# Optimization experiments

Measured on AMD Instinct MI355X. Metric: run time of the kernel, lower is better.

Reference implementation:

```python
import jax, jax.numpy as jnp
import numpy as np

B, N, FEAT, MSG, LINK_H, CLS = 8, 128, 1024, 256, 512, 600
PROP = 2  # propagate_layers


def setup_inputs() -> dict:
    key = jax.random.key(0)
    ks = jax.random.split(key, 16)
    g = lambda k, shape, s=0.02: jax.random.normal(k, shape, dtype=jnp.float32) * s
    inp = {
        'edge_features': g(ks[0], (B, N, N, FEAT), 1.0),
        'node_features': g(ks[1], (B, N, FEAT), 1.0),
        'adj_mat': jnp.zeros((B, N, N), jnp.float32),          # shape placeholder only
        'node_labels': jnp.zeros((B, N, CLS), jnp.float32),    # shape placeholder only
        'human_nums': 64,
        'obj_nums': 64,
        # feature resize linears (Linear(FEAT -> MSG))
        'W_er': g(ks[2], (MSG, FEAT)), 'b_er': jnp.zeros((MSG,), jnp.float32),
        'W_nr': g(ks[3], (MSG, FEAT)), 'b_nr': jnp.zeros((MSG,), jnp.float32),
        # link fun (GraphConv): 1x1 Conv2d(MSG->LINK_H), ReLU, 1x1 Conv2d(LINK_H->1)
        'W_l1': g(ks[4], (LINK_H, MSG)), 'b_l1': jnp.zeros((LINK_H,), jnp.float32),
        'W_l2': g(ks[5], (1, LINK_H)), 'b_l2': jnp.zeros((1,), jnp.float32),
        # message fun linear_concat_relu: Linear(node+edge = 2*MSG -> MSG), ReLU
        'W_m': g(ks[6], (MSG, 2 * MSG)), 'b_m': jnp.zeros((MSG,), jnp.float32),
        # GRU(input=MSG, hidden=MSG), single layer single step
        'W_ih': g(ks[7], (3 * MSG, MSG)), 'b_ih': jnp.zeros((3 * MSG,), jnp.float32),
        'W_hh': g(ks[8], (3 * MSG, MSG)), 'b_hh': jnp.zeros((3 * MSG,), jnp.float32),
        # readout fc: Linear(MSG -> CLS)
        'W_r': g(ks[9], (CLS, MSG)), 'b_r': jnp.zeros((CLS,), jnp.float32),
    }
    return inp


def reference(edge_features, node_features, adj_mat, node_labels,
              human_nums, obj_nums,
              W_er, b_er, W_nr, b_nr, W_l1, b_l1, W_l2, b_l2,
              W_m, b_m, W_ih, b_ih, W_hh, b_hh, W_r, b_r):
    # valid_node_num = human_nums + obj_nums == N for every batch element.
    # Resize raw features to message size.
    e = edge_features @ W_er.T + b_er        # [B, v, w, MSG]
    h = node_features @ W_nr.T + b_nr        # [B, w, MSG]  (node states are never rewritten in source)
    # Split concat-linear into two matmuls to avoid materializing [B,N,N,2*MSG].
    W_mh, W_me = W_m[:, :MSG], W_m[:, MSG:]
    msg_h = jnp.einsum('bwd,md->bwm', h, W_mh)                 # node part, shared over target v
    msg_e = jnp.einsum('bvwd,md->bvwm', e, W_me) + b_m          # edge part (original e, constant over rounds)
    edge_state = e
    m = None
    pred_adj = None
    for _ in range(PROP):
        # link fun: per-(v,w) MLP over channels (1x1 convs)
        x = jax.nn.relu(edge_state @ W_l1.T + b_l1)             # [B,v,w,LINK_H]
        pred_adj = (x @ W_l2.T + b_l2)[..., 0]                  # [B,N,N]
        sig = jax.nn.sigmoid(pred_adj)
        # message fun linear_concat_relu, gated by predicted adjacency
        m = jax.nn.relu(msg_h[:, None, :, :] + msg_e)           # [B,v,w,MSG]
        m = sig[..., None] * m
        # hidden_edge_states[round+1][:, :, w, v] = m_v[:, :, w]
        edge_state = jnp.swapaxes(m, 1, 2)
    # node update happens per node each round but hidden node states are never
    # written back in the source, so only the last round's GRU step matters.
    m_sum = m.sum(axis=2)                                       # [B,v,MSG]
    gi = m_sum @ W_ih.T + b_ih
    gh = h @ W_hh.T + b_hh
    ir, iz, inn = jnp.split(gi, 3, axis=-1)
    hr, hz, hn = jnp.split(gh, 3, axis=-1)
    r = jax.nn.sigmoid(ir + hr)
    z = jax.nn.sigmoid(iz + hz)
    n = jnp.tanh(inn + r * hn)
    h_new = (1.0 - z) * n + z * h                               # [B,N,MSG]
    pred_node_labels = h_new @ W_r.T + b_r                      # [B,N,CLS]
    return pred_adj, pred_node_labels
```

## Files before the change

### kernel.cpp

```cpp
#include <hip/hip_runtime.h>
#include <cstdint>
#include <cstddef>

#define NND   128
#define FEATD 1024
#define MSGD  256
#define LHD   512
#define CLSD  600
#define LDST  264

typedef __bf16 bf16_t;
typedef bf16_t bf16x8 __attribute__((ext_vector_type(8)));
typedef float  f32x4  __attribute__((ext_vector_type(4)));
typedef unsigned short u16;
typedef u16 u16x8 __attribute__((ext_vector_type(8)));
typedef u16 u16x4 __attribute__((ext_vector_type(4)));

static __device__ __forceinline__ float bf2f(u16 u) {
  union { unsigned u; float f; } x; x.u = ((unsigned)u) << 16; return x.f;
}
static __device__ __forceinline__ u16 f2bf(float f) {
  union { float f; unsigned u; } x; x.f = f;
  return (u16)((x.u + 0x7fffu + ((x.u >> 16) & 1u)) >> 16);
}
static __device__ __forceinline__ f32x4 mfma16(u16x8 a, u16x8 b, f32x4 c) {
  return __builtin_amdgcn_mfma_f32_16x16x32_bf16(
      __builtin_bit_cast(bf16x8, a), __builtin_bit_cast(bf16x8, b), c, 0, 0, 0);
}
static __device__ __forceinline__ f32x4 zero4() {
  f32x4 v; v[0] = 0.f; v[1] = 0.f; v[2] = 0.f; v[3] = 0.f; return v;
}
static __device__ __forceinline__ float sigm(float x) { return 1.0f / (1.0f + expf(-x)); }

__global__ void k_cvt(const float* __restrict__ src, u16* __restrict__ dst, int n) {
  int i = (blockIdx.x * 256 + threadIdx.x) * 4;
  if (i + 3 < n) {
    float4 f = *(const float4*)(src + i);
    u16x4 o; o[0] = f2bf(f.x); o[1] = f2bf(f.y); o[2] = f2bf(f.z); o[3] = f2bf(f.w);
    *(u16x4*)(dst + i) = o;
  }
}

__global__ __launch_bounds__(256) void k_comb(const float* __restrict__ Wm,
                                              const float* __restrict__ Wer,
                                              const float* __restrict__ b_er,
                                              const float* __restrict__ b_m,
                                              u16* __restrict__ WcombB,
                                              float* __restrict__ bcomb) {
  const int m = blockIdx.x >> 2, ch = blockIdx.x & 3;
  const int d = ch * 256 + threadIdx.x;
  float s = 0.f;
  for (int k = 0; k < 256; ++k)
    s += Wm[(size_t)m * 512 + 256 + k] * Wer[(size_t)k * FEATD + d];
  WcombB[(size_t)m * FEATD + d] = f2bf(s);
  if (ch == 0 && threadIdx.x == 0) {
    float bb2 = b_m[m];
    for (int k = 0; k < 256; ++k) bb2 += Wm[(size_t)m * 512 + 256 + k] * b_er[k];
    bcomb[m] = bb2;
  }
}

__global__ __launch_bounds__(256) void s1_hmsg(const float* __restrict__ node,
                                               const float* __restrict__ Wnr,
                                               const float* __restrict__ bnr,
                                               const float* __restrict__ Wm,
                                               float* __restrict__ h32,
                                               u16* __restrict__ msghB) {
  __shared__ float nrow[FEATD];
  __shared__ float hrow[MSGD];
  const int r = blockIdx.x;
  const int t = threadIdx.x;
  *(float4*)(&nrow[t * 4]) = *(const float4*)(node + (size_t)r * FEATD + t * 4);
  __syncthreads();
  float acc = bnr[t];
  for (int d = 0; d < FEATD; ++d) acc += nrow[d] * Wnr[(size_t)t * FEATD + d];
  h32[(size_t)r * MSGD + t] = acc;
  hrow[t] = acc;
  __syncthreads();
  float mh = 0.f;
  for (int k = 0; k < MSGD; ++k) mh += hrow[k] * Wm[(size_t)t * 2 * MSGD + k];
  msghB[(size_t)r * MSGD + t] = f2bf(mh);
}

__global__ __launch_bounds__(256, 2) void k_main(
    const float* __restrict__ edge, const u16* __restrict__ Wer, const u16* __restrict__ Wm,
    const u16* __restrict__ Wl1, const float* __restrict__ b_er, const float* __restrict__ b_m,
    const float* __restrict__ b_l1, const float* __restrict__ W_l2, const float* __restrict__ b_l2,
    const u16* __restrict__ msgh, u16* __restrict__ M0g, float* __restrict__ pa_out) {
  __shared__ __align__(16) u16 lsE[64][LDST];
  __shared__ __align__(16) u16 lsM[64][LDST];
  __shared__ float lsPA[4][64];
  __shared__ float lsSig[64];

  const int tid = threadIdx.x, lane = tid & 63, wave = tid >> 6;
  const int lh = lane & 15, lq = lane >> 4;
  const int base = blockIdx.x * 64;
  const int bb = base >> 14, vv = (base >> 7) & 127, w0 = base & 127;

  f32x4 acc[4][4];
#pragma unroll
  for (int m = 0; m < 4; ++m)
#pragma unroll
    for (int t = 0; t < 4; ++t) acc[m][t] = zero4();

  const int srow = tid >> 2;
  const int scq  = (tid & 3) * 16;
  const float* esrc = edge + (size_t)(base + srow) * FEATD + scq;
  float4 lda[4], ldb[4];

  auto LOADS_A = [&](int s) {
#pragma unroll
    for (int i = 0; i < 4; ++i) lda[i] = *(const float4*)(esrc + s * 64 + i * 4);
  };
  auto LOADS_B = [&](int s) {
#pragma unroll
    for (int i = 0; i < 4; ++i) ldb[i] = *(const float4*)(esrc + s * 64 + i * 4);
  };
  auto WRITES = [&](const float4* ld, int slot) {
    u16* wp = &lsE[srow][slot * 64 + scq];
    u16x8 o0, o1;
    o0[0] = f2bf(ld[0].x); o0[1] = f2bf(ld[0].y); o0[2] = f2bf(ld[0].z); o0[3] = f2bf(ld[0].w);
    o0[4] = f2bf(ld[1].x); o0[5] = f2bf(ld[1].y); o0[6] = f2bf(ld[1].z); o0[7] = f2bf(ld[1].w);
    o1[0] = f2bf(ld[2].x); o1[1] = f2bf(ld[2].y); o1[2] = f2bf(ld[2].z); o1[3] = f2bf(ld[2].w);
    o1[4] = f2bf(ld[3].x); o1[5] = f2bf(ld[3].y); o1[6] = f2bf(ld[3].z); o1[7] = f2bf(ld[3].w);
    *(u16x8*)wp = o0;
    *(u16x8*)(wp + 8) = o1;
  };
  auto MSTEP = [&](int sk, int slot) {
#pragma unroll
    for (int ks = 0; ks < 2; ++ks) {
      u16x8 afr[4];
#pragma unroll
      for (int m = 0; m < 4; ++m)
        afr[m] = *(const u16x8*)(&lsE[16 * m + lh][slot * 64 + ks * 32 + lq * 8]);
      const int kg = sk * 64 + ks * 32 + lq * 8;
#pragma unroll
      for (int t = 0; t < 4; ++t) {
        int col = wave * 64 + t * 16 + lh;
        u16x8 bfr = *(const u16x8*)(Wer + (size_t)col * FEATD + kg);
#pragma unroll
        for (int m = 0; m < 4; ++m) acc[m][t] = mfma16(afr[m], bfr, acc[m][t]);
      }
    }
  };

  LOADS_A(0);
  LOADS_B(1);
  for (int s2 = 0; s2 < 16; s2 += 2) {
    WRITES(lda, 0);
    if (s2 + 2 < 16) LOADS_A(s2 + 2);
    __syncthreads();
    MSTEP(s2, 0);
    WRITES(ldb, 1);
    if (s2 + 3 < 16) LOADS_B(s2 + 3);
    __syncthreads();
    MSTEP(s2 + 1, 1);
  }
  __syncthreads();
#pragma unroll
  for (int t = 0; t < 4; ++t) {
    int col = wave * 64 + t * 16 + lh;
    float be = b_er[col];
#pragma unroll
    for (int m = 0; m < 4; ++m)
#pragma unroll
      for (int j = 0; j < 4; ++j)
        lsE[16 * m + 4 * lq + j][col] = f2bf(acc[m][t][j] + be);
  }
  __syncthreads();

  float prow[4][4];
#pragma unroll
  for (int m = 0; m < 4; ++m)
#pragma unroll
    for (int j = 0; j < 4; ++j) prow[m][j] = 0.f;
#pragma unroll
  for (int np = 0; np < 2; ++np) {
#pragma unroll
    for (int m = 0; m < 4; ++m)
#pragma unroll
      for (int t = 0; t < 4; ++t) acc[m][t] = zero4();
#pragma unroll
    for (int ks = 0; ks < 8; ++ks) {
      u16x8 afr[4];
#pragma unroll
      for (int m = 0; m < 4; ++m) afr[m] = *(const u16x8*)(&lsE[16 * m + lh][ks * 32 + lq * 8]);
      const int kg = ks * 32 + lq * 8;
#pragma unroll
      for (int t = 0; t < 4; ++t) {
        int col = wave * 128 + np * 64 + t * 16 + lh;
        u16x8 bfr = *(const u16x8*)(Wl1 + (size_t)col * MSGD + kg);
#pragma unroll
        for (int m = 0; m < 4; ++m) acc[m][t] = mfma16(afr[m], bfr, acc[m][t]);
      }
    }
#pragma unroll
    for (int t = 0; t < 4; ++t) {
      int col = wave * 128 + np * 64 + t * 16 + lh;
      float bl = b_l1[col], wl = W_l2[col];
#pragma unroll
      for (int m = 0; m < 4; ++m)
#pragma unroll
        for (int j = 0; j < 4; ++j) prow[m][j] += fmaxf(acc[m][t][j] + bl, 0.f) * wl;
    }
  }
#pragma unroll
  for (int off = 1; off < 16; off <<= 1)
#pragma unroll
    for (int m = 0; m < 4; ++m)
#pragma unroll
      for (int j = 0; j < 4; ++j) prow[m][j] += __shfl_xor(prow[m][j], off, 64);
  if (lh == 0) {
#pragma unroll
    for (int m = 0; m < 4; ++m)
#pragma unroll
      for (int j = 0; j < 4; ++j) lsPA[wave][16 * m + 4 * lq + j] = prow[m][j];
  }
  __syncthreads();
  if (tid < 64) {
    float pa1 = lsPA[0][tid] + lsPA[1][tid] + lsPA[2][tid] + lsPA[3][tid] + b_l2[0];
    lsSig[tid] = sigm(pa1);
  }
#pragma unroll
  for (int i = 0; i < 8; ++i) {
    int idx = tid + i * 256;
    int row = idx >> 5;
    int c8 = (idx & 31) << 3;
    *(u16x8*)(&lsM[row][c8]) =
        *(const u16x8*)(msgh + (size_t)(bb * NND + w0 + row) * MSGD + c8);
  }
  __syncthreads();

#pragma unroll
  for (int m = 0; m < 4; ++m)
#pragma unroll
    for (int t = 0; t < 4; ++t) acc[m][t] = zero4();
#pragma unroll
  for (int ks = 0; ks < 8; ++ks) {
    u16x8 afr[4];
#pragma unroll
    for (int m = 0; m < 4; ++m) afr[m] = *(const u16x8*)(&lsE[16 * m + lh][ks * 32 + lq * 8]);
    const int kg = ks * 32 + lq * 8;
#pragma unroll
    for (int t = 0; t < 4; ++t) {
      int col = wave * 64 + t * 16 + lh;
      u16x8 bfr = *(const u16x8*)(Wm + (size_t)col * 512 + 256 + kg);
#pragma unroll
      for (int m = 0; m < 4; ++m) acc[m][t] = mfma16(afr[m], bfr, acc[m][t]);
    }
  }
#pragma unroll
  for (int t = 0; t < 4; ++t) {
    int col = wave * 64 + t * 16 + lh;
    float bm = b_m[col];
#pragma unroll
    for (int m = 0; m < 4; ++m)
#pragma unroll
      for (int j = 0; j < 4; ++j) {
        int row = 16 * m + 4 * lq + j;
        float mh = bf2f(lsM[row][col]);
        lsM[row][col] = f2bf(fmaxf(acc[m][t][j] + bm + mh, 0.f));
      }
  }
  __syncthreads();
#pragma unroll
  for (int i = 0; i < 8; ++i) {
    int idx = tid + i * 256;
    int row = idx >> 5;
    int c8 = (idx & 31) << 3;
    u16x8 m0v = *(const u16x8*)(&lsM[row][c8]);
    if (M0g) *(u16x8*)(M0g + (size_t)(base + row) * MSGD + c8) = m0v;
    float s = lsSig[row];
    u16x8 sc;
#pragma unroll
    for (int j = 0; j < 8; ++j) sc[j] = f2bf(bf2f(m0v[j]) * s);
    *(u16x8*)(&lsM[row][c8]) = sc;
  }
  __syncthreads();

#pragma unroll
  for (int m = 0; m < 4; ++m)
#pragma unroll
    for (int j = 0; j < 4; ++j) prow[m][j] = 0.f;
#pragma unroll
  for (int np = 0; np < 2; ++np) {
#pragma unroll
    for (int m = 0; m < 4; ++m)
#pragma unroll
      for (int t = 0; t < 4; ++t) acc[m][t] = zero4();
#pragma unroll
    for (int ks = 0; ks < 8; ++ks) {
      u16x8 afr[4];
#pragma unroll
      for (int m = 0; m < 4; ++m) afr[m] = *(const u16x8*)(&lsM[16 * m + lh][ks * 32 + lq * 8]);
      const int kg = ks * 32 + lq * 8;
#pragma unroll
      for (int t = 0; t < 4; ++t) {
        int col = wave * 128 + np * 64 + t * 16 + lh;
        u16x8 bfr = *(const u16x8*)(Wl1 + (size_t)col * MSGD + kg);
#pragma unroll
        for (int m = 0; m < 4; ++m) acc[m][t] = mfma16(afr[m], bfr, acc[m][t]);
      }
    }
#pragma unroll
    for (int t = 0; t < 4; ++t) {
      int col = wave * 128 + np * 64 + t * 16 + lh;
      float bl = b_l1[col], wl = W_l2[col];
#pragma unroll
      for (int m = 0; m < 4; ++m)
#pragma unroll
        for (int j = 0; j < 4; ++j) prow[m][j] += fmaxf(acc[m][t][j] + bl, 0.f) * wl;
    }
  }
#pragma unroll
  for (int off = 1; off < 16; off <<= 1)
#pragma unroll
    for (int m = 0; m < 4; ++m)
#pragma unroll
      for (int j = 0; j < 4; ++j) prow[m][j] += __shfl_xor(prow[m][j], off, 64);
  if (lh == 0) {
#pragma unroll
    for (int m = 0; m < 4; ++m)
#pragma unroll
      for (int j = 0; j < 4; ++j) lsPA[wave][16 * m + 4 * lq + j] = prow[m][j];
  }
  __syncthreads();
  if (tid < 64) {
    float q = lsPA[0][tid] + lsPA[1][tid] + lsPA[2][tid] + lsPA[3][tid] + b_l2[0];
    size_t o = ((size_t)bb * NND + (w0 + tid)) * NND + vv;
    pa_out[o] = q;
  }
}

__global__ __launch_bounds__(256) void k_msum_lite(const u16* __restrict__ M0g,
                                                   const float* __restrict__ qv,
                                                   float* __restrict__ msum) {
  __shared__ float sig[128];
  const int bv = blockIdx.x, tid = threadIdx.x;
  if (tid < 128) sig[tid] = sigm(qv[(size_t)bv * NND + tid]);
  __syncthreads();
  const u16* p = M0g + (size_t)bv * NND * MSGD + tid;
  float a = 0.f;
#pragma unroll 8
  for (int w = 0; w < 128; ++w) a += sig[w] * bf2f(p[(size_t)w * MSGD]);
  msum[(size_t)bv * MSGD + tid] = a;
}

__global__ __launch_bounds__(256, 2) void k_msum2(
    const float* __restrict__ edge, const u16* __restrict__ Wcomb,
    const float* __restrict__ bcomb, const u16* __restrict__ msgh,
    const float* __restrict__ qv, float* __restrict__ msum) {
  __shared__ __align__(16) u16 lsE[64][LDST];
  __shared__ __align__(16) u16 lsM[64][LDST];
  __shared__ float lsSig[64];
  const int tid = threadIdx.x, lane = tid & 63, wave = tid >> 6;
  const int lh = lane & 15, lq = lane >> 4;
  const int bv = blockIdx.x;
  const int bb = bv >> 7;

  float csum[4] = {0.f, 0.f, 0.f, 0.f};

  for (int hh = 0; hh < 2; ++hh) {
    if (tid < 64) lsSig[tid] = sigm(qv[(size_t)bv * NND + hh * 64 + tid]);
#pragma unroll
    for (int i = 0; i < 8; ++i) {
      int idx = tid + i * 256;
      int row = idx >> 5;
      int c8 = (idx & 31) << 3;
      *(u16x8*)(&lsM[row][c8]) =
          *(const u16x8*)(msgh + (size_t)(bb * NND + hh * 64 + row) * MSGD + c8);
    }
    f32x4 acc[4][4];
#pragma unroll
    for (int m = 0; m < 4; ++m)
#pragma unroll
      for (int t = 0; t < 4; ++t) acc[m][t] = zero4();

    for (int kc = 0; kc < 4; ++kc) {
#pragma unroll
      for (int i = 0; i < 16; ++i) {
        int idx = tid + i * 256;
        int row = idx >> 6;
        int c4 = (idx & 63) << 2;
        float4 f = *(const float4*)(edge + (size_t)(bv * NND + hh * 64 + row) * FEATD + kc * 256 + c4);
        u16x4 o; o[0] = f2bf(f.x); o[1] = f2bf(f.y); o[2] = f2bf(f.z); o[3] = f2bf(f.w);
        *(u16x4*)(&lsE[row][c4]) = o;
      }
      __syncthreads();
#pragma unroll
      for (int ks = 0; ks < 8; ++ks) {
        u16x8 afr[4];
#pragma unroll
        for (int m = 0; m < 4; ++m) afr[m] = *(const u16x8*)(&lsE[16 * m + lh][ks * 32 + lq * 8]);
        const int kg = kc * 256 + ks * 32 + lq * 8;
#pragma unroll
        for (int t = 0; t < 4; ++t) {
          int col = wave * 64 + t * 16 + lh;
          u16x8 bfr = *(const u16x8*)(Wcomb + (size_t)col * FEATD + kg);
#pragma unroll
          for (int m = 0; m < 4; ++m) acc[m][t] = mfma16(afr[m], bfr, acc[m][t]);
        }
      }
      __syncthreads();
    }
#pragma unroll
    for (int t = 0; t < 4; ++t) {
      int col = wave * 64 + t * 16 + lh;
      float bc = bcomb[col];
#pragma unroll
      for (int m = 0; m < 4; ++m)
#pragma unroll
        for (int j = 0; j < 4; ++j) {
          int row = 16 * m + 4 * lq + j;
          float m0 = fmaxf(acc[m][t][j] + bc + bf2f(lsM[row][col]), 0.f);
          csum[t] += lsSig[row] * m0;
        }
    }
    __syncthreads();
  }
#pragma unroll
  for (int off = 16; off < 64; off <<= 1)
#pragma unroll
    for (int t = 0; t < 4; ++t) csum[t] += __shfl_xor(csum[t], off, 64);
  if (lq == 0) {
#pragma unroll
    for (int t = 0; t < 4; ++t)
      msum[(size_t)bv * MSGD + wave * 64 + t * 16 + lh] = csum[t];
  }
}

__global__ __launch_bounds__(256) void k_gru(const float* __restrict__ msum,
                                             const float* __restrict__ h32,
                                             const float* __restrict__ Wih, const float* __restrict__ bih,
                                             const float* __restrict__ Whh, const float* __restrict__ bhh,
                                             const float* __restrict__ Wr, const float* __restrict__ br,
                                             float* __restrict__ outlab) {
  __shared__ __align__(16) float sM[8][256];
  __shared__ __align__(16) float sH[8][256];
  __shared__ __align__(16) float sHn[8][256];
  const int tid = threadIdx.x;
  const int r0 = blockIdx.x * 8;
#pragma unroll
  for (int i = 0; i < 2; ++i) {
    int idx = tid + i * 256;
    int row = idx >> 6;
    int c = (idx & 63) << 2;
    *(float4*)(&sM[row][c]) = *(const float4*)(msum + (size_t)(r0 + row) * 256 + c);
    *(float4*)(&sH[row][c]) = *(const float4*)(h32 + (size_t)(r0 + row) * 256 + c);
  }
  __syncthreads();
  float gi[3][8], gh[3][8];
#pragma unroll
  for (int c = 0; c < 3; ++c) {
    float bi_ = bih[tid + 256 * c], bh_ = bhh[tid + 256 * c];
#pragma unroll
    for (int rr = 0; rr < 8; ++rr) { gi[c][rr] = bi_; gh[c][rr] = bh_; }
  }
  for (int k = 0; k < 256; k += 4) {
    float4 wi[3], wh[3];
#pragma unroll
    for (int c = 0; c < 3; ++c) {
      wi[c] = *(const float4*)(Wih + (size_t)(tid + 256 * c) * 256 + k);
      wh[c] = *(const float4*)(Whh + (size_t)(tid + 256 * c) * 256 + k);
    }
#pragma unroll
    for (int rr = 0; rr < 8; ++rr) {
      float4 ms = *(const float4*)(&sM[rr][k]);
      float4 hh = *(const float4*)(&sH[rr][k]);
#pragma unroll
      for (int c = 0; c < 3; ++c) {
        gi[c][rr] += wi[c].x * ms.x + wi[c].y * ms.y + wi[c].z * ms.z + wi[c].w * ms.w;
        gh[c][rr] += wh[c].x * hh.x + wh[c].y * hh.y + wh[c].z * hh.z + wh[c].w * hh.w;
      }
    }
  }
#pragma unroll
  for (int rr = 0; rr < 8; ++rr) {
    float r = sigm(gi[0][rr] + gh[0][rr]);
    float z = sigm(gi[1][rr] + gh[1][rr]);
    float n = tanhf(gi[2][rr] + r * gh[2][rr]);
    sHn[rr][tid] = (1.f - z) * n + z * sH[rr][tid];
  }
  __syncthreads();
  float lab[3][8];
  int cs[3]; bool has[3];
#pragma unroll
  for (int c = 0; c < 3; ++c) {
    cs[c] = tid + 256 * c;
    has[c] = cs[c] < CLSD;
    float b0 = has[c] ? br[cs[c]] : 0.f;
#pragma unroll
    for (int rr = 0; rr < 8; ++rr) lab[c][rr] = b0;
  }
  for (int k = 0; k < 256; k += 4) {
    float4 wr[3];
#pragma unroll
    for (int c = 0; c < 3; ++c) {
      if (has[c]) wr[c] = *(const float4*)(Wr + (size_t)cs[c] * 256 + k);
      else { wr[c].x = 0.f; wr[c].y = 0.f; wr[c].z = 0.f; wr[c].w = 0.f; }
    }
#pragma unroll
    for (int rr = 0; rr < 8; ++rr) {
      float4 hv = *(const float4*)(&sHn[rr][k]);
#pragma unroll
      for (int c = 0; c < 3; ++c)
        lab[c][rr] += wr[c].x * hv.x + wr[c].y * hv.y + wr[c].z * hv.z + wr[c].w * hv.w;
    }
  }
#pragma unroll
  for (int c = 0; c < 3; ++c) {
    if (has[c]) {
#pragma unroll
      for (int rr = 0; rr < 8; ++rr)
        outlab[(size_t)(r0 + rr) * CLSD + cs[c]] = lab[c][rr];
    }
  }
}

extern "C" void kernel_launch(void* const* d_in, const int* in_sizes, int n_in,
                              void* d_out, int out_size, void* d_ws, size_t ws_size,
                              hipStream_t stream) {
  const float* edge = (const float*)d_in[0];
  const float* node = (const float*)d_in[1];
  const float* W_er = (const float*)d_in[6];
  const float* b_er = (const float*)d_in[7];
  const float* W_nr = (const float*)d_in[8];
  const float* b_nr = (const float*)d_in[9];
  const float* W_l1 = (const float*)d_in[10];
  const float* b_l1 = (const float*)d_in[11];
  const float* W_l2 = (const float*)d_in[12];
  const float* b_l2 = (const float*)d_in[13];
  const float* W_m  = (const float*)d_in[14];
  const float* b_m  = (const float*)d_in[15];
  const float* W_ih = (const float*)d_in[16];
  const float* b_ih = (const float*)d_in[17];
  const float* W_hh = (const float*)d_in[18];
  const float* b_hh = (const float*)d_in[19];
  const float* W_r  = (const float*)d_in[20];
  const float* b_r  = (const float*)d_in[21];

  char* ws = (char*)d_ws;
  size_t off = 0;
  auto alloc = [&](size_t bytes) -> void* {
    void* p = ws + off;
    off += (bytes + 511) & ~(size_t)511;
    return p;
  };
  u16* WerB     = (u16*)alloc((size_t)262144 * 2);
  u16* WmB      = (u16*)alloc((size_t)131072 * 2);
  u16* Wl1B     = (u16*)alloc((size_t)131072 * 2);
  u16* WcombB   = (u16*)alloc((size_t)262144 * 2);
  float* bcombF = (float*)alloc((size_t)256 * 4);
  u16* msghB    = (u16*)alloc((size_t)262144 * 2);
  float* h32    = (float*)alloc((size_t)262144 * 4);
  float* msum   = (float*)alloc((size_t)262144 * 4);
  u16* M0g      = (u16*)alloc((size_t)33554432 * 2);
  size_t off_m0 = off;
  const bool fast = (ws_size >= off_m0);
  u16* M0arg = fast ? M0g : (u16*)nullptr;

  float* out_pa  = (float*)d_out;
  float* out_lab = out_pa + 131072;

  k_cvt  <<<256,  256, 0, stream>>>(W_er, WerB, 262144);
  k_cvt  <<<128,  256, 0, stream>>>(W_m,  WmB,  131072);
  k_cvt  <<<128,  256, 0, stream>>>(W_l1, Wl1B, 131072);
  s1_hmsg<<<1024, 256, 0, stream>>>(node, W_nr, b_nr, W_m, h32, msghB);
  if (!fast)
    k_comb<<<1024, 256, 0, stream>>>(W_m, W_er, b_er, b_m, WcombB, bcombF);

  k_main<<<2048, 256, 0, stream>>>(edge, WerB, WmB, Wl1B, b_er, b_m, b_l1, W_l2, b_l2,
                                   msghB, M0arg, out_pa);
  if (fast)
    k_msum_lite<<<1024, 256, 0, stream>>>(M0g, out_pa, msum);
  else
    k_msum2<<<1024, 256, 0, stream>>>(edge, WcombB, bcombF, msghB, out_pa, msum);
  k_gru<<<128, 256, 0, stream>>>(msum, h32, W_ih, b_ih, W_hh, b_hh, W_r, b_r, out_lab);
}
```

Baseline: 715.3 us.

## Move node resize and message-h to MFMA kernels, transpose GRU weights, vectorize msum

Replaces the scalar per-row node resize and msg_h kernel with two bf16 MFMA GEMM kernels, converting W_nr to bf16 first. The GRU/readout weights are pre-transposed so each thread reads coalesced columns instead of strided rows. The msum reduction now uses 16-byte vector loads with an LDS partial-sum combine. These target the small side kernels around the main edge kernel. They add extra conversion launches and bf16 rounding of h for msg_h.

After: 806.1 us. 1.13x slower.

```diff
diff --git a/kernel.cpp b/kernel.cpp
--- a/kernel.cpp
+++ b/kernel.cpp
@@ -38,6 +38,27 @@
     float4 f = *(const float4*)(src + i);
     u16x4 o; o[0] = f2bf(f.x); o[1] = f2bf(f.y); o[2] = f2bf(f.z); o[3] = f2bf(f.w);
     *(u16x4*)(dst + i) = o;
+  }
+}
+
+__global__ __launch_bounds__(256) void k_cvtT(const float* __restrict__ in,
+                                              float* __restrict__ out, int R) {
+  __shared__ float tile[32][33];
+  const int tx = threadIdx.x & 31, ty = threadIdx.x >> 5;
+  const int tr = blockIdx.x >> 3, tc = blockIdx.x & 7;
+#pragma unroll
+  for (int i = 0; i < 4; ++i) {
+    int r = tr * 32 + ty + i * 8;
+    if (r < R) tile[ty + i * 8][tx] = in[(size_t)r * 256 + tc * 32 + tx];
+  }
+  __syncthreads();
+  const int r = tr * 32 + tx;
+  if (r < R) {
+#pragma unroll
+    for (int i = 0; i < 4; ++i) {
+      int c = tc * 32 + ty + i * 8;
+      out[(size_t)c * R + r] = tile[tx][ty + i * 8];
+    }
   }
 }
 
@@ -60,29 +81,114 @@
   }
 }
 
-__global__ __launch_bounds__(256) void s1_hmsg(const float* __restrict__ node,
-                                               const float* __restrict__ Wnr,
-                                               const float* __restrict__ bnr,
-                                               const float* __restrict__ Wm,
-                                               float* __restrict__ h32,
-                                               u16* __restrict__ msghB) {
-  __shared__ float nrow[FEATD];
-  __shared__ float hrow[MSGD];
-  const int r = blockIdx.x;
-  const int t = threadIdx.x;
-  *(float4*)(&nrow[t * 4]) = *(const float4*)(node + (size_t)r * FEATD + t * 4);
-  __syncthreads();
-  float acc = bnr[t];
-  for (int d = 0; d < FEATD; ++d) acc += nrow[d] * Wnr[(size_t)t * FEATD + d];
-  h32[(size_t)r * MSGD + t] = acc;
-  hrow[t] = acc;
-  __syncthreads();
-  float mh = 0.f;
-  for (int k = 0; k < MSGD; ++k) mh += hrow[k] * Wm[(size_t)t * 2 * MSGD + k];
-  msghB[(size_t)r * MSGD + t] = f2bf(mh);
-}
-
-__global__ __launch_bounds__(256, 2) void k_main(
+__global__ __launch_bounds__(256) void k_h(const float* __restrict__ node,
+                                           const u16* __restrict__ Wnr,
+                                           const float* __restrict__ bnr,
+                                           float* __restrict__ h32,
+                                           u16* __restrict__ hbf) {
+  __shared__ __align__(16) u16 lsA[64][LDST];
+  const int tid = threadIdx.x, lane = tid & 63, wave = tid >> 6;
+  const int lh = lane & 15, lq = lane >> 4;
+  const int base = blockIdx.x * 64;
+
+  f32x4 acc[4][4];
+#pragma unroll
+  for (int m = 0; m < 4; ++m)
+#pragma unroll
+    for (int t = 0; t < 4; ++t) acc[m][t] = zero4();
+
+  for (int kc = 0; kc < 4; ++kc) {
+#pragma unroll
+    for (int i = 0; i < 16; ++i) {
+      int idx = tid + i * 256;
+      int row = idx >> 6;
+      int c4 = (idx & 63) << 2;
+      float4 f = *(const float4*)(node + (size_t)(base + row) * FEATD + kc * 256 + c4);
+      u16x4 o; o[0] = f2bf(f.x); o[1] = f2bf(f.y); o[2] = f2bf(f.z); o[3] = f2bf(f.w);
+      *(u16x4*)(&lsA[row][c4]) = o;
+    }
+    __syncthreads();
+#pragma unroll
+    for (int ks = 0; ks < 8; ++ks) {
+      u16x8 afr[4];
+#pragma unroll
+      for (int m = 0; m < 4; ++m) afr[m] = *(const u16x8*)(&lsA[16 * m + lh][ks * 32 + lq * 8]);
+      const int kg = kc * 256 + ks * 32 + lq * 8;
+#pragma unroll
+      for (int t = 0; t < 4; ++t) {
+        int col = wave * 64 + t * 16 + lh;
+        u16x8 bfr = *(const u16x8*)(Wnr + (size_t)col * FEATD + kg);
+#pragma unroll
+        for (int m = 0; m < 4; ++m) acc[m][t] = mfma16(afr[m], bfr, acc[m][t]);
+      }
+    }
+    __syncthreads();
+  }
+#pragma unroll
+  for (int t = 0; t < 4; ++t) {
+    int col = wave * 64 + t * 16 + lh;
+    float be = bnr[col];
+#pragma unroll
+    for (int m = 0; m < 4; ++m)
+#pragma unroll
+      for (int j = 0; j < 4; ++j) {
+        int row = 16 * m + 4 * lq + j;
+        float v = acc[m][t][j] + be;
+        size_t o = (size_t)(base + row) * MSGD + col;
+        h32[o] = v; hbf[o] = f2bf(v);
+      }
+  }
+}
+
+__global__ __launch_bounds__(256) void k_msgh(const u16* __restrict__ hbf,
+                                              const u16* __restrict__ Wm,
+                                              u16* __restrict__ msgh) {
+  __shared__ __align__(16) u16 lsA[64][LDST];
+  const int tid = threadIdx.x, lane = tid & 63, wave = tid >> 6;
+  const int lh = lane & 15, lq = lane >> 4;
+  const int base = blockIdx.x * 64;
+
+#pragma unroll
+  for (int i = 0; i < 8; ++i) {
+    int idx = tid + i * 256;
+    int row = idx >> 5;
+    int c8 = (idx & 31) << 3;
+    *(u16x8*)(&lsA[row][c8]) = *(const u16x8*)(hbf + (size_t)(base + row) * MSGD + c8);
+  }
+  __syncthreads();
+  f32x4 acc[4][4];
+#pragma unroll
+  for (int m = 0; m < 4; ++m)
+#pragma unroll
+    for (int t = 0; t < 4; ++t) acc[m][t] = zero4();
+#pragma unroll
+  for (int ks = 0; ks < 8; ++ks) {
+    u16x8 afr[4];
+#pragma unroll
+    for (int m = 0; m < 4; ++m) afr[m] = *(const u16x8*)(&lsA[16 * m + lh][ks * 32 + lq * 8]);
+    const int kg = ks * 32 + lq * 8;
+#pragma unroll
+    for (int t = 0; t < 4; ++t) {
+      int col = wave * 64 + t * 16 + lh;
+      u16x8 bfr = *(const u16x8*)(Wm + (size_t)col * 512 + kg);
+#pragma unroll
+      for (int m = 0; m < 4; ++m) acc[m][t] = mfma16(afr[m], bfr, acc[m][t]);
+    }
+  }
+#pragma unroll
+  for (int t = 0; t < 4; ++t) {
+    int col = wave * 64 + t * 16 + lh;
+#pragma unroll
+    for (int m = 0; m < 4; ++m)
+#pragma unroll
+      for (int j = 0; j < 4; ++j) {
+        int row = 16 * m + 4 * lq + j;
+        msgh[(size_t)(base + row) * MSGD + col] = f2bf(acc[m][t][j]);
+      }
+  }
+}
+
+__global__ __launch_bounds__(256, 2) void k_main_full(
     const float* __restrict__ edge, const u16* __restrict__ Wer, const u16* __restrict__ Wm,
     const u16* __restrict__ Wl1, const float* __restrict__ b_er, const float* __restrict__ b_m,
     const float* __restrict__ b_l1, const float* __restrict__ W_l2, const float* __restrict__ b_l2,
@@ -336,14 +442,28 @@
                                                    const float* __restrict__ qv,
                                                    float* __restrict__ msum) {
   __shared__ float sig[128];
+  __shared__ __align__(16) float part[8][256];
   const int bv = blockIdx.x, tid = threadIdx.x;
   if (tid < 128) sig[tid] = sigm(qv[(size_t)bv * NND + tid]);
   __syncthreads();
-  const u16* p = M0g + (size_t)bv * NND * MSGD + tid;
-  float a = 0.f;
-#pragma unroll 8
-  for (int w = 0; w < 128; ++w) a += sig[w] * bf2f(p[(size_t)w * MSGD]);
-  msum[(size_t)bv * MSGD + tid] = a;
+  const int cg = (tid & 31) * 8, rg = tid >> 5;
+  float a[8];
+#pragma unroll
+  for (int j = 0; j < 8; ++j) a[j] = 0.f;
+  for (int i = 0; i < 16; ++i) {
+    int row = rg + i * 8;
+    u16x8 v = *(const u16x8*)(M0g + ((size_t)bv * NND + row) * MSGD + cg);
+    float s = sig[row];
+#pragma unroll
+    for (int j = 0; j < 8; ++j) a[j] += s * bf2f(v[j]);
+  }
+#pragma unroll
+  for (int j = 0; j < 8; ++j) part[rg][cg + j] = a[j];
+  __syncthreads();
+  float r = 0.f;
+#pragma unroll
+  for (int g = 0; g < 8; ++g) r += part[g][tid];
+  msum[(size_t)bv * MSGD + tid] = r;
 }
 
 __global__ __launch_bounds__(256, 2) void k_msum2(
@@ -429,12 +549,15 @@
   }
 }
 
-__global__ __launch_bounds__(256) void k_gru(const float* __restrict__ msum,
-                                             const float* __restrict__ h32,
-                                             const float* __restrict__ Wih, const float* __restrict__ bih,
-                                             const float* __restrict__ Whh, const float* __restrict__ bhh,
-                                             const float* __restrict__ Wr, const float* __restrict__ br,
-                                             float* __restrict__ outlab) {
+__global__ __launch_bounds__(256) void k_gru_t(const float* __restrict__ msum,
+                                               const float* __restrict__ h32,
+                                               const float* __restrict__ WihT,
+                                               const float* __restrict__ bih,
+                                               const float* __restrict__ WhhT,
+                                               const float* __restrict__ bhh,
+                                               const float* __restrict__ WrT,
+                                               const float* __restrict__ br,
+                                               float* __restrict__ outlab) {
   __shared__ __align__(16) float sM[8][256];
   __shared__ __align__(16) float sH[8][256];
   __shared__ __align__(16) float sHn[8][256];
@@ -456,22 +579,18 @@
 #pragma unroll
     for (int rr = 0; rr < 8; ++rr) { gi[c][rr] = bi_; gh[c][rr] = bh_; }
   }
-  for (int k = 0; k < 256; k += 4) {
-    float4 wi[3], wh[3];
-#pragma unroll
-    for (int c = 0; c < 3; ++c) {
-      wi[c] = *(const float4*)(Wih + (size_t)(tid + 256 * c) * 256 + k);
-      wh[c] = *(const float4*)(Whh + (size_t)(tid + 256 * c) * 256 + k);
-    }
+  for (int k = 0; k < 256; ++k) {
+    float wi0 = WihT[(size_t)k * 768 + tid];
+    float wi1 = WihT[(size_t)k * 768 + 256 + tid];
+    float wi2 = WihT[(size_t)k * 768 + 512 + tid];
+    float wh0 = WhhT[(size_t)k * 768 + tid];
+    float wh1 = WhhT[(size_t)k * 768 + 256 + tid];
+    float wh2 = WhhT[(size_t)k * 768 + 512 + tid];
 #pragma unroll
     for (int rr = 0; rr < 8; ++rr) {
-      float4 ms = *(const float4*)(&sM[rr][k]);
-      float4 hh = *(const float4*)(&sH[rr][k]);
-#pragma unroll
-      for (int c = 0; c < 3; ++c) {
-        gi[c][rr] += wi[c].x * ms.x + wi[c].y * ms.y + wi[c].z * ms.z + wi[c].w * ms.w;
-        gh[c][rr] += wh[c].x * hh.x + wh[c].y * hh.y + wh[c].z * hh.z + wh[c].w * hh.w;
-      }
+      float ms = sM[rr][k], hh = sH[rr][k];
+      gi[0][rr] += wi0 * ms; gi[1][rr] += wi1 * ms; gi[2][rr] += wi2 * ms;
+      gh[0][rr] += wh0 * hh; gh[1][rr] += wh1 * hh; gh[2][rr] += wh2 * hh;
     }
   }
 #pragma unroll
@@ -483,37 +602,30 @@
   }
   __syncthreads();
   float lab[3][8];
-  int cs[3]; bool has[3];
+  const bool has2 = (tid + 512) < CLSD;
 #pragma unroll
   for (int c = 0; c < 3; ++c) {
-    cs[c] = tid + 256 * c;
-    has[c] = cs[c] < CLSD;
-    float b0 = has[c] ? br[cs[c]] : 0.f;
+    int cs = tid + 256 * c;
+    float b0 = (c < 2 || has2) ? br[cs < CLSD ? cs : 0] : 0.f;
+    if (c < 2) b0 = br[cs];
 #pragma unroll
     for (int rr = 0; rr < 8; ++rr) lab[c][rr] = b0;
   }
-  for (int k = 0; k < 256; k += 4) {
-    float4 wr[3];
-#pragma unroll
-    for (int c = 0; c < 3; ++c) {
-      if (has[c]) wr[c] = *(const float4*)(Wr + (size_t)cs[c] * 256 + k);
-      else { wr[c].x = 0.f; wr[c].y = 0.f; wr[c].z = 0.f; wr[c].w = 0.f; }
-    }
+  for (int k = 0; k < 256; ++k) {
+    float w0 = WrT[(size_t)k * CLSD + tid];
+    float w1 = WrT[(size_t)k * CLSD + 256 + tid];
+    float w2 = has2 ? WrT[(size_t)k * CLSD + 512 + tid] : 0.f;
 #pragma unroll
     for (int rr = 0; rr < 8; ++rr) {
-      float4 hv = *(const float4*)(&sHn[rr][k]);
-#pragma unroll
-      for (int c = 0; c < 3; ++c)
-        lab[c][rr] += wr[c].x * hv.x + wr[c].y * hv.y + wr[c].z * hv.z + wr[c].w * hv.w;
-    }
-  }
-#pragma unroll
-  for (int c = 0; c < 3; ++c) {
-    if (has[c]) {
-#pragma unroll
-      for (int rr = 0; rr < 8; ++rr)
-        outlab[(size_t)(r0 + rr) * CLSD + cs[c]] = lab[c][rr];
-    }
+      float hv = sHn[rr][k];
+      lab[0][rr] += w0 * hv; lab[1][rr] += w1 * hv; lab[2][rr] += w2 * hv;
+    }
+  }
+#pragma unroll
+  for (int rr = 0; rr < 8; ++rr) {
+    outlab[(size_t)(r0 + rr) * CLSD + tid] = lab[0][rr];
+    outlab[(size_t)(r0 + rr) * CLSD + 256 + tid] = lab[1][rr];
+    if (has2) outlab[(size_t)(r0 + rr) * CLSD + 512 + tid] = lab[2][rr];
   }
 }
 
@@ -547,13 +659,18 @@
     return p;
   };
   u16* WerB     = (u16*)alloc((size_t)262144 * 2);
+  u16* WnrB     = (u16*)alloc((size_t)262144 * 2);
   u16* WmB      = (u16*)alloc((size_t)131072 * 2);
   u16* Wl1B     = (u16*)alloc((size_t)131072 * 2);
   u16* WcombB   = (u16*)alloc((size_t)262144 * 2);
   float* bcombF = (float*)alloc((size_t)256 * 4);
   u16* msghB    = (u16*)alloc((size_t)262144 * 2);
+  u16* hB       = (u16*)alloc((size_t)262144 * 2);
   float* h32    = (float*)alloc((size_t)262144 * 4);
   float* msum   = (float*)alloc((size_t)262144 * 4);
+  float* WihT   = (float*)alloc((size_t)196608 * 4);
+  float* WhhT   = (float*)alloc((size_t)196608 * 4);
+  float* WrT    = (float*)alloc((size_t)153600 * 4);
   u16* M0g      = (u16*)alloc((size_t)33554432 * 2);
   size_t off_m0 = off;
   const bool fast = (ws_size >= off_m0);
@@ -562,18 +679,23 @@
   float* out_pa  = (float*)d_out;
   float* out_lab = out_pa + 131072;
 
-  k_cvt  <<<256,  256, 0, stream>>>(W_er, WerB, 262144);
-  k_cvt  <<<128,  256, 0, stream>>>(W_m,  WmB,  131072);
-  k_cvt  <<<128,  256, 0, stream>>>(W_l1, Wl1B, 131072);
-  s1_hmsg<<<1024, 256, 0, stream>>>(node, W_nr, b_nr, W_m, h32, msghB);
+  k_cvt  <<<256, 256, 0, stream>>>(W_er, WerB, 262144);
+  k_cvt  <<<256, 256, 0, stream>>>(W_nr, WnrB, 262144);
+  k_cvt  <<<128, 256, 0, stream>>>(W_m,  WmB,  131072);
+  k_cvt  <<<128, 256, 0, stream>>>(W_l1, Wl1B, 131072);
+  k_cvtT <<<192, 256, 0, stream>>>(W_ih, WihT, 768);
+  k_cvtT <<<192, 256, 0, stream>>>(W_hh, WhhT, 768);
+  k_cvtT <<<152, 256, 0, stream>>>(W_r,  WrT,  600);
+  k_h    <<<16,  256, 0, stream>>>(node, WnrB, b_nr, h32, hB);
+  k_msgh <<<16,  256, 0, stream>>>(hB, WmB, msghB);
   if (!fast)
     k_comb<<<1024, 256, 0, stream>>>(W_m, W_er, b_er, b_m, WcombB, bcombF);
 
-  k_main<<<2048, 256, 0, stream>>>(edge, WerB, WmB, Wl1B, b_er, b_m, b_l1, W_l2, b_l2,
-                                   msghB, M0arg, out_pa);
+  k_main_full<<<2048, 256, 0, stream>>>(edge, WerB, WmB, Wl1B, b_er, b_m, b_l1, W_l2, b_l2,
+                                        msghB, M0arg, out_pa);
   if (fast)
     k_msum_lite<<<1024, 256, 0, stream>>>(M0g, out_pa, msum);
   else
     k_msum2<<<1024, 256, 0, stream>>>(edge, WcombB, bcombF, msghB, out_pa, msum);
-  k_gru<<<128, 256, 0, stream>>>(msum, h32, W_ih, b_ih, W_hh, b_hh, W_r, b_r, out_lab);
-}
+  k_gru_t<<<128, 256, 0, stream>>>(msum, h32, WihT, b_ih, WhhT, b_hh, WrT, b_r, out_lab);
+}
```
